# Kernel optimization log

Hardware: AMD Instinct MI355X
Metric: run time of the kernel (lower is better)

The kernel has to match this reference:

```python
import jax, jax.numpy as jnp
import numpy as np

N_EMBD, N_HEAD, N_KV_HEAD = 1024, 16, 4
HEAD_DIM = N_EMBD // N_HEAD  # 64
VE_GATE_CH = 12
RMS_EPS = 1.1920929e-07  # torch fp32 finfo.eps (F.rms_norm default)


def setup_inputs() -> dict:
    key = jax.random.key(0)
    ks = jax.random.split(key, 8)
    B, S = 2, 2048
    x = jax.random.normal(ks[0], (B, S, N_EMBD), dtype=jnp.float32)
    ve = jax.random.normal(ks[1], (B, S, N_KV_HEAD * HEAD_DIM), dtype=jnp.float32)
    # RoPE cache
    half = HEAD_DIM // 2
    inv_freq = 1.0 / (10000.0 ** (np.arange(half, dtype=np.float32) / half))
    ang = np.arange(S, dtype=np.float32)[:, None] * inv_freq[None, :]  # [S, 32]
    cos = jnp.asarray(np.cos(ang))[:, None, :]  # [S,1,32]
    sin = jnp.asarray(np.sin(ang))[:, None, :]
    attention_mask = jnp.ones((B, S), dtype=jnp.int32)
    sc = 0.02
    Wq = sc * jax.random.normal(ks[2], (N_EMBD, N_EMBD), dtype=jnp.float32)
    Wk = sc * jax.random.normal(ks[3], (N_KV_HEAD * HEAD_DIM, N_EMBD), dtype=jnp.float32)
    Wv = sc * jax.random.normal(ks[4], (N_KV_HEAD * HEAD_DIM, N_EMBD), dtype=jnp.float32)
    Wproj = sc * jax.random.normal(ks[5], (N_EMBD, N_EMBD), dtype=jnp.float32)
    Wgate = sc * jax.random.normal(ks[6], (N_KV_HEAD, VE_GATE_CH), dtype=jnp.float32)
    return {"x": x, "ve": ve, "cos": cos, "sin": sin,
            "Wq": Wq, "Wk": Wk, "Wv": Wv, "Wproj": Wproj, "Wgate": Wgate,
            "attention_mask": attention_mask, "left_window": 1024}


def _rope(t, cos, sin):
    half = t.shape[-1] // 2
    t1, t2 = t[..., :half], t[..., half:]
    return jnp.concatenate([t1 * cos + t2 * sin, -t1 * sin + t2 * cos], axis=-1)


def _rms_norm(t):
    return t * jax.lax.rsqrt(jnp.mean(t * t, axis=-1, keepdims=True) + RMS_EPS)


def reference(x, ve, cos, sin, Wq, Wk, Wv, Wproj, Wgate, attention_mask, left_window):
    B, S, _ = x.shape
    q = (x @ Wq.T).reshape(B, S, N_HEAD, HEAD_DIM)
    k = (x @ Wk.T).reshape(B, S, N_KV_HEAD, HEAD_DIM)
    v = (x @ Wv.T).reshape(B, S, N_KV_HEAD, HEAD_DIM)
    # value-embedding gating: 3*sigmoid(linear(x[..., :12])) per kv head
    gate = 3.0 * jax.nn.sigmoid(x[..., :VE_GATE_CH] @ Wgate.T)  # [B,S,Hkv]
    v = v + gate[..., None] * ve.reshape(B, S, N_KV_HEAD, HEAD_DIM)
    q = _rms_norm(_rope(q, cos, sin)) * 1.2
    k = _rms_norm(_rope(k, cos, sin)) * 1.2
    q = q.transpose(0, 2, 1, 3)  # [B,H,S,hd]
    k = k.transpose(0, 2, 1, 3)  # [B,Hkv,S,hd]
    v = v.transpose(0, 2, 1, 3)
    rep = N_HEAD // N_KV_HEAD
    k = jnp.repeat(k, rep, axis=1)  # repeat_interleave over head dim
    v = jnp.repeat(v, rep, axis=1)
    # causal + sliding-window bias, materialized as in the original
    pos = jnp.arange(S)
    allowed = (pos[:, None] >= pos[None, :]) & ((pos[:, None] - pos[None, :]) < left_window)
    allowed = allowed[None, None] & attention_mask.astype(bool)[:, None, None, :]  # [B,1,S,S]
    neg = jnp.finfo(x.dtype).min
    bias = jnp.where(allowed, jnp.float32(0.0), neg).astype(x.dtype)
    scale = 1.0 / np.sqrt(HEAD_DIM)
    scores = jnp.einsum('bhqd,bhkd->bhqk', q, k) * scale + bias
    w = jax.nn.softmax(scores, axis=-1)
    y = jnp.einsum('bhqk,bhkd->bhqd', w, v)
    y = y.transpose(0, 2, 1, 3).reshape(B, S, N_EMBD)
    return y @ Wproj.T
```

## Files before the change

kernel.cpp:

```cpp
#include <hip/hip_runtime.h>
#include <hip/hip_bf16.h>

#define SS 2048
#define EE 1024
#define RMS_EPS 1.1920929e-07f

typedef short v8s __attribute__((ext_vector_type(8)));
typedef float v4f __attribute__((ext_vector_type(4)));

#define MFMA16 __builtin_amdgcn_mfma_f32_16x16x32_bf16

__device__ __forceinline__ ushort f2bf(float f){
    union { __hip_bfloat16 b; ushort u; } c; c.b = __float2bfloat16(f); return c.u;
}
__device__ __forceinline__ float bf2f(ushort u){
    union { uint u; float f; } c; c.u = ((uint)u) << 16; return c.f;
}
__device__ __forceinline__ void split8(const float* p, uint4& H, uint4& L){
    float4 a = *(const float4*)p, b = *(const float4*)(p+4);
    float v[8] = {a.x,a.y,a.z,a.w,b.x,b.y,b.z,b.w};
    ushort hs[8], ls[8];
#pragma unroll
    for (int e=0;e<8;e++){
        ushort h = f2bf(v[e]);
        hs[e] = h;
        ls[e] = f2bf(v[e] - bf2f(h));
    }
    H = *(uint4*)hs; L = *(uint4*)ls;
}

__global__ __launch_bounds__(256)
void split_pre(const float* __restrict__ s, ushort* __restrict__ dh,
               ushort* __restrict__ dl, int n8)
{
    int i = blockIdx.x*256 + threadIdx.x;
    if (i < n8){
        uint4 H, L;
        split8(s + (size_t)i*8, H, L);
        *(uint4*)(dh + (size_t)i*8) = H;
        *(uint4*)(dl + (size_t)i*8) = L;
    }
}

template<bool PRE>
__global__ __launch_bounds__(256)
void qkv_kernel(const float* __restrict__ x, const float* __restrict__ ve,
                const float* __restrict__ Wq, const float* __restrict__ Wk,
                const float* __restrict__ Wv, const float* __restrict__ Wg,
                const ushort* __restrict__ xh, const ushort* __restrict__ xl,
                const ushort* __restrict__ Wch, const ushort* __restrict__ Wcl,
                const float* __restrict__ cosb, const float* __restrict__ sinb,
                ushort* __restrict__ qhb, ushort* __restrict__ qlb,
                ushort* __restrict__ khb, ushort* __restrict__ klb,
                ushort* __restrict__ vhT, ushort* __restrict__ vlT)
{
    __shared__ ushort Axh[128*64];
    __shared__ ushort Axl[128*64];
    __shared__ ushort Bwh[64*64];
    __shared__ ushort Bwl[64*64];
    const int t = threadIdx.x;
    const int lane = t & 63, w = t >> 6;
    const int g = lane >> 4, ln = lane & 15;
    const int nt = blockIdx.x, mt = blockIdx.y;
    const float* W;
    if (nt < 16)      W = Wq + (size_t)nt*64*EE;
    else if (nt < 20) W = Wk + (size_t)(nt-16)*64*EE;
    else              W = Wv + (size_t)(nt-20)*64*EE;
    const v4f vzero = {0.f,0.f,0.f,0.f};
    v4f acc[2][4];
#pragma unroll
    for (int m=0;m<2;m++)
#pragma unroll
        for (int j=0;j<4;j++) acc[m][j] = vzero;

    const int sr = t>>3, sc = t&7;
    for (int kt = 0; kt < EE; kt += 64){
#pragma unroll
        for (int p2=0;p2<4;p2++){
            int rr = sr + 32*p2;
            int off = rr*64 + ((sc ^ (rr&7))<<3);
            if (PRE){
                *(uint4*)&Axh[off] = *(const uint4*)(xh + (size_t)(mt*128+rr)*EE + kt + sc*8);
                *(uint4*)&Axl[off] = *(const uint4*)(xl + (size_t)(mt*128+rr)*EE + kt + sc*8);
            } else {
                uint4 H,L; split8(x + (size_t)(mt*128+rr)*EE + kt + sc*8, H, L);
                *(uint4*)&Axh[off] = H; *(uint4*)&Axl[off] = L;
            }
        }
#pragma unroll
        for (int p2=0;p2<2;p2++){
            int rr = sr + 32*p2;
            int off = rr*64 + ((sc ^ (rr&7))<<3);
            if (PRE){
                *(uint4*)&Bwh[off] = *(const uint4*)(Wch + (size_t)(nt*64+rr)*EE + kt + sc*8);
                *(uint4*)&Bwl[off] = *(const uint4*)(Wcl + (size_t)(nt*64+rr)*EE + kt + sc*8);
            } else {
                uint4 H,L; split8(W + (size_t)rr*EE + kt + sc*8, H, L);
                *(uint4*)&Bwh[off] = H; *(uint4*)&Bwl[off] = L;
            }
        }
        __syncthreads();
        v8s ah[2][2], al[2][2], bh[4][2], bl[4][2];
#pragma unroll
        for (int m=0;m<2;m++){
            int row = 32*w + 16*m + ln;
#pragma unroll
            for (int s=0;s<2;s++){
                int off = row*64 + (((4*s+g) ^ (row&7))<<3);
                ah[m][s] = *(v8s*)&Axh[off];
                al[m][s] = *(v8s*)&Axl[off];
            }
        }
#pragma unroll
        for (int j=0;j<4;j++){
            int row = 16*j + ln;
#pragma unroll
            for (int s=0;s<2;s++){
                int off = row*64 + (((4*s+g) ^ (row&7))<<3);
                bh[j][s] = *(v8s*)&Bwh[off];
                bl[j][s] = *(v8s*)&Bwl[off];
            }
        }
#pragma unroll
        for (int m=0;m<2;m++)
#pragma unroll
            for (int j=0;j<4;j++)
#pragma unroll
                for (int s=0;s<2;s++){
                    acc[m][j] = MFMA16(ah[m][s], bh[j][s], acc[m][j], 0,0,0);
                    acc[m][j] = MFMA16(ah[m][s], bl[j][s], acc[m][j], 0,0,0);
                    acc[m][j] = MFMA16(al[m][s], bh[j][s], acc[m][j], 0,0,0);
                }
        __syncthreads();
    }

#pragma unroll
    for (int m=0;m<2;m++){
#pragma unroll
        for (int r=0;r<4;r++){
            int srow = mt*128 + 32*w + 16*m + 4*g + r;
            int bb  = srow >> 11;
            int ss_ = srow & 2047;
            float v0 = acc[m][0][r], v1 = acc[m][1][r];
            float v2 = acc[m][2][r], v3 = acc[m][3][r];
            if (nt < 20){
                float c0 = cosb[ss_*32 + ln],      s0 = sinb[ss_*32 + ln];
                float c1 = cosb[ss_*32 + 16 + ln], s1 = sinb[ss_*32 + 16 + ln];
                float lo0 =  v0*c0 + v2*s0, hi0 = -v0*s0 + v2*c0;
                float lo1 =  v1*c1 + v3*s1, hi1 = -v1*s1 + v3*c1;
                float ssq = lo0*lo0 + hi0*hi0 + lo1*lo1 + hi1*hi1;
                ssq += __shfl_xor(ssq, 1); ssq += __shfl_xor(ssq, 2);
                ssq += __shfl_xor(ssq, 4); ssq += __shfl_xor(ssq, 8);
                float rs = rsqrtf(ssq*(1.f/64.f) + RMS_EPS) * 1.2f;
                size_t base = (nt < 16) ? ((size_t)(bb*16 + nt)*SS + ss_)*64
                                        : ((size_t)(bb*4 + (nt-16))*SS + ss_)*64;
                ushort* dh = (nt < 16) ? (qhb + base) : (khb + base);
                ushort* dl = (nt < 16) ? (qlb + base) : (klb + base);
                float o0 = lo0*rs, o1 = lo1*rs, o2 = hi0*rs, o3 = hi1*rs;
                ushort h0 = f2bf(o0), h1 = f2bf(o1), h2 = f2bf(o2), h3 = f2bf(o3);
                dh[ln]    = h0; dl[ln]    = f2bf(o0 - bf2f(h0));
                dh[16+ln] = h1; dl[16+ln] = f2bf(o1 - bf2f(h1));
                dh[32+ln] = h2; dl[32+ln] = f2bf(o2 - bf2f(h2));
                dh[48+ln] = h3; dl[48+ln] = f2bf(o3 - bf2f(h3));
            } else {
                int head = nt - 20;
                float gsum = 0.f;
                const float* xr = x + (size_t)srow * EE;
#pragma unroll
                for (int c = 0; c < 12; c++) gsum += xr[c] * Wg[head*12 + c];
                float gate = 3.f / (1.f + __expf(-gsum));
                const float* ver = ve + (size_t)srow*256 + head*64;
                size_t vbase = ((size_t)(bb*4 + head)*64)*SS + ss_;
                float dv[4] = {v0, v1, v2, v3};
#pragma unroll
                for (int j=0;j<4;j++){
                    int d = 16*j + ln;
                    float ov = dv[j] + gate*ver[d];
                    ushort hh = f2bf(ov);
                    vhT[vbase + (size_t)d*SS] = hh;
                    vlT[vbase + (size_t)d*SS] = f2bf(ov - bf2f(hh));
                }
            }
        }
    }
}

__global__ __launch_bounds__(256)
void attn_kernel(const ushort* __restrict__ qhb, const ushort* __restrict__ qlb,
                 const ushort* __restrict__ khb, const ushort* __restrict__ klb,
                 const ushort* __restrict__ vhT, const ushort* __restrict__ vlT,
                 const int* __restrict__ amask, const int* __restrict__ lwp,
                 ushort* __restrict__ yhb, ushort* __restrict__ ylb)
{
    __shared__ ushort SMEM[16384];
    __shared__ float mbias[64];
    ushort* Kh = SMEM;
    ushort* Kl = SMEM + 4096;
    ushort* Vh = SMEM + 8192;
    ushort* Vl = SMEM + 12288;
    const int t = threadIdx.x, lane = t & 63, w = t >> 6;
    const int g = lane >> 4, ln = lane & 15;
    const int qt = blockIdx.x, bh = blockIdx.y;
    const int b = bh >> 4, h = bh & 15, kvh = h >> 2;
    const int LW = lwp[0];
    const int q0 = qt*64;
    const ushort* Qhp = qhb + ((size_t)(b*16+h)*SS + q0)*64;
    const ushort* Qlp = qlb + ((size_t)(b*16+h)*SS + q0)*64;
    const ushort* Khp = khb + ((size_t)(b*4+kvh)*SS)*64;
    const ushort* Klp = klb + ((size_t)(b*4+kvh)*SS)*64;
    const ushort* Vhp = vhT + (size_t)(b*4+kvh)*64*SS;
    const ushort* Vlp = vlT + (size_t)(b*4+kvh)*64*SS;

    v8s qfh[2], qfl[2];
    {
        int row = 16*w + ln;
#pragma unroll
        for (int s=0;s<2;s++){
            qfh[s] = *(const v8s*)(Qhp + (size_t)row*64 + (4*s+g)*8);
            qfl[s] = *(const v8s*)(Qlp + (size_t)row*64 + (4*s+g)*8);
        }
    }
    const int qg = q0 + 16*w + ln;
    const int keyk = (ln&3) ^ ((ln>>2)<<1);
    float m_r = -1e30f, l_r = 0.f;
    const v4f vzero = {0.f,0.f,0.f,0.f};
    v4f o[4];
#pragma unroll
    for (int dt=0;dt<4;dt++) o[dt] = vzero;

    const int sr = t>>3, sc = t&7;
    int lo = q0 - LW + 1; if (lo < 0) lo = 0;
    for (int kt = lo>>6; kt <= qt; kt++){
        int k0 = kt*64;
        __syncthreads();
#pragma unroll
        for (int p2=0;p2<2;p2++){
            int rr = sr + 32*p2;
            int kkey = (rr&3) ^ (((rr>>3)&3)<<1);
            int koff = rr*64 + ((sc ^ kkey)<<3);
            *(uint4*)&Kh[koff] = *(const uint4*)(Khp + (size_t)(k0+rr)*64 + sc*8);
            *(uint4*)&Kl[koff] = *(const uint4*)(Klp + (size_t)(k0+rr)*64 + sc*8);
            int voff = rr*64 + ((sc ^ (rr&7))<<3);
            *(uint4*)&Vh[voff] = *(const uint4*)(Vhp + (size_t)rr*SS + k0 + sc*8);
            *(uint4*)&Vl[voff] = *(const uint4*)(Vlp + (size_t)rr*SS + k0 + sc*8);
        }
        if (t < 64) mbias[t] = amask[(b<<11) + k0 + t] ? 0.f : -3.0e38f;
        __syncthreads();

        float p[4][4];
#pragma unroll
        for (int tau=0;tau<4;tau++){
            v4f sa = vzero;
            int krow = 32*(tau&1) + 8*(ln>>2) + 4*(tau>>1) + (ln&3);
#pragma unroll
            for (int s=0;s<2;s++){
                int off = krow*64 + (((4*s+g) ^ keyk)<<3);
                v8s afh = *(v8s*)&Kh[off];
                v8s afl = *(v8s*)&Kl[off];
                sa = MFMA16(afh, qfh[s], sa, 0,0,0);
                sa = MFMA16(afh, qfl[s], sa, 0,0,0);
                sa = MFMA16(afl, qfh[s], sa, 0,0,0);
            }
#pragma unroll
            for (int r=0;r<4;r++) p[tau][r] = sa[r];
        }

        float pmax = -3.0e38f;
#pragma unroll
        for (int tau=0;tau<4;tau++)
#pragma unroll
            for (int r=0;r<4;r++){
                int kk  = 32*(tau&1) + 8*g + 4*(tau>>1) + r;
                int kgl = k0 + kk;
                float scv = p[tau][r]*0.125f + mbias[kk];
                bool ok = (kgl <= qg) && (qg - kgl < LW);
                scv = ok ? scv : -3.0e38f;
                p[tau][r] = scv;
                pmax = fmaxf(pmax, scv);
            }
        pmax = fmaxf(pmax, __shfl_xor(pmax,16));
        pmax = fmaxf(pmax, __shfl_xor(pmax,32));
        float mnew = fmaxf(m_r, pmax);
        float al = __expf(m_r - mnew);
        float ls = 0.f;
#pragma unroll
        for (int tau=0;tau<4;tau++)
#pragma unroll
            for (int r=0;r<4;r++){
                float e = __expf(p[tau][r] - mnew);
                p[tau][r] = e; ls += e;
            }
        ls += __shfl_xor(ls,16); ls += __shfl_xor(ls,32);
        m_r = mnew; l_r = l_r*al + ls;

        v8s pbh[2], pbl[2];
#pragma unroll
        for (int s=0;s<2;s++){
            v8s ph, pl;
#pragma unroll
            for (int e=0;e<8;e++){
                float val = p[2*(e>>2)+s][e&3];
                ushort hh = f2bf(val);
                ph[e] = (short)hh;
                pl[e] = (short)f2bf(val - bf2f(hh));
            }
            pbh[s]=ph; pbl[s]=pl;
        }
#pragma unroll
        for (int dt=0;dt<4;dt++){
            o[dt] = o[dt]*al;
            int drow = 16*dt + ln;
#pragma unroll
            for (int s=0;s<2;s++){
                int off = drow*64 + (((4*s+g) ^ (ln&7))<<3);
                v8s vfh = *(v8s*)&Vh[off];
                v8s vfl = *(v8s*)&Vl[off];
                o[dt] = MFMA16(vfh, pbh[s], o[dt], 0,0,0);
                o[dt] = MFMA16(vfh, pbl[s], o[dt], 0,0,0);
                o[dt] = MFMA16(vfl, pbh[s], o[dt], 0,0,0);
            }
        }
    }

    __syncthreads();
    float inv = (l_r > 0.f) ? (1.0f / l_r) : 0.f;
    float* Ot = (float*)SMEM;
#pragma unroll
    for (int dt=0;dt<4;dt++)
#pragma unroll
        for (int r=0;r<4;r++){
            int d = 16*dt + 4*g + r;
            Ot[d*68 + 16*w + ln] = o[dt][r]*inv;
        }
    __syncthreads();
    {
        int q = t>>2, dp = t&3;
        ushort th[16], tl[16];
#pragma unroll
        for (int i=0;i<16;i++){
            float val = Ot[(dp*16+i)*68 + q];
            ushort hh = f2bf(val);
            th[i] = hh;
            tl[i] = f2bf(val - bf2f(hh));
        }
        size_t doff = (size_t)(b*SS + q0 + q)*EE + h*64 + dp*16;
        *(uint4*)(yhb + doff)     = *(uint4*)&th[0];
        *(uint4*)(yhb + doff + 8) = *(uint4*)&th[8];
        *(uint4*)(ylb + doff)     = *(uint4*)&tl[0];
        *(uint4*)(ylb + doff + 8) = *(uint4*)&tl[8];
    }
}

template<bool PRE>
__global__ __launch_bounds__(256)
void proj_kernel(const ushort* __restrict__ yhb, const ushort* __restrict__ ylb,
                 const float* __restrict__ Wp, const ushort* __restrict__ Wph,
                 const ushort* __restrict__ Wpl, float* __restrict__ out)
{
    __shared__ ushort Ayh[128*64];
    __shared__ ushort Ayl[128*64];
    __shared__ ushort Bh[64*64];
    __shared__ ushort Bl[64*64];
    const int t = threadIdx.x;
    const int lane = t & 63, w = t >> 6;
    const int g = lane >> 4, ln = lane & 15;
    const int nt = blockIdx.x, mt = blockIdx.y;
    const v4f vzero = {0.f,0.f,0.f,0.f};
    v4f acc[2][4];
#pragma unroll
    for (int m=0;m<2;m++)
#pragma unroll
        for (int j=0;j<4;j++) acc[m][j] = vzero;

    const int sr = t>>3, sc = t&7;
    for (int kt = 0; kt < EE; kt += 64){
#pragma unroll
        for (int p2=0;p2<4;p2++){
            int rr = sr + 32*p2;
            int off = rr*64 + ((sc ^ (rr&7))<<3);
            *(uint4*)&Ayh[off] = *(const uint4*)(yhb + (size_t)(mt*128+rr)*EE + kt + sc*8);
            *(uint4*)&Ayl[off] = *(const uint4*)(ylb + (size_t)(mt*128+rr)*EE + kt + sc*8);
        }
#pragma unroll
        for (int p2=0;p2<2;p2++){
            int rr = sr + 32*p2;
            int off = rr*64 + ((sc ^ (rr&7))<<3);
            if (PRE){
                *(uint4*)&Bh[off] = *(const uint4*)(Wph + (size_t)(nt*64+rr)*EE + kt + sc*8);
                *(uint4*)&Bl[off] = *(const uint4*)(Wpl + (size_t)(nt*64+rr)*EE + kt + sc*8);
            } else {
                uint4 H,L; split8(Wp + (size_t)(nt*64+rr)*EE + kt + sc*8, H, L);
                *(uint4*)&Bh[off] = H; *(uint4*)&Bl[off] = L;
            }
        }
        __syncthreads();
        v8s ah[2][2], al[2][2], bh[4][2], bl[4][2];
#pragma unroll
        for (int m=0;m<2;m++){
            int row = 32*w + 16*m + ln;
#pragma unroll
            for (int s=0;s<2;s++){
                int off = row*64 + (((4*s+g) ^ (row&7))<<3);
                ah[m][s] = *(v8s*)&Ayh[off];
                al[m][s] = *(v8s*)&Ayl[off];
            }
        }
#pragma unroll
        for (int j=0;j<4;j++){
            int row = 16*j + ln;
#pragma unroll
            for (int s=0;s<2;s++){
                int off = row*64 + (((4*s+g) ^ (row&7))<<3);
                bh[j][s] = *(v8s*)&Bh[off];
                bl[j][s] = *(v8s*)&Bl[off];
            }
        }
#pragma unroll
        for (int m=0;m<2;m++)
#pragma unroll
            for (int j=0;j<4;j++)
#pragma unroll
                for (int s=0;s<2;s++){
                    acc[m][j] = MFMA16(ah[m][s], bh[j][s], acc[m][j], 0,0,0);
                    acc[m][j] = MFMA16(ah[m][s], bl[j][s], acc[m][j], 0,0,0);
                    acc[m][j] = MFMA16(al[m][s], bh[j][s], acc[m][j], 0,0,0);
                }
        __syncthreads();
    }

#pragma unroll
    for (int m=0;m<2;m++)
#pragma unroll
        for (int r=0;r<4;r++){
            size_t grow = (size_t)mt*128 + 32*w + 16*m + 4*g + r;
#pragma unroll
            for (int j=0;j<4;j++)
                out[grow*EE + nt*64 + 16*j + ln] = acc[m][j][r];
        }
}

extern "C" void kernel_launch(void* const* d_in, const int* in_sizes, int n_in,
                              void* d_out, int out_size, void* d_ws, size_t ws_size,
                              hipStream_t stream)
{
    (void)in_sizes; (void)n_in; (void)out_size;
    const float* x     = (const float*)d_in[0];
    const float* ve    = (const float*)d_in[1];
    const float* cosb  = (const float*)d_in[2];
    const float* sinb  = (const float*)d_in[3];
    const float* Wq    = (const float*)d_in[4];
    const float* Wk    = (const float*)d_in[5];
    const float* Wv    = (const float*)d_in[6];
    const float* Wp    = (const float*)d_in[7];
    const float* Wg    = (const float*)d_in[8];
    const int*   amask = (const int*)d_in[9];
    const int*   lw    = (const int*)d_in[10];
    float* out = (float*)d_out;
    char* ws = (char*)d_ws;

    if (ws_size >= (size_t)(50u<<20)){
        ushort* xh  = (ushort*)(ws);
        ushort* xl  = (ushort*)(ws + ( 8u<<20));
        ushort* Wch = (ushort*)(ws + (16u<<20));
        ushort* Wcl = (ushort*)(ws + (19u<<20));
        ushort* Wph = (ushort*)(ws + (22u<<20));
        ushort* Wpl = (ushort*)(ws + (24u<<20));
        ushort* qhb = (ushort*)(ws + (26u<<20));
        ushort* qlb = (ushort*)(ws + (34u<<20));
        ushort* khb = (ushort*)(ws + (42u<<20));
        ushort* klb = (ushort*)(ws + (44u<<20));
        ushort* vhT = (ushort*)(ws + (46u<<20));
        ushort* vlT = (ushort*)(ws + (48u<<20));
        ushort* yhb = xh;
        ushort* ylb = xl;

        split_pre<<<2048, 256, 0, stream>>>(x,  xh,  xl,  524288);
        split_pre<<< 512, 256, 0, stream>>>(Wq, Wch, Wcl, 131072);
        split_pre<<< 128, 256, 0, stream>>>(Wk, Wch + (size_t)1024*EE, Wcl + (size_t)1024*EE, 32768);
        split_pre<<< 128, 256, 0, stream>>>(Wv, Wch + (size_t)1280*EE, Wcl + (size_t)1280*EE, 32768);
        split_pre<<< 512, 256, 0, stream>>>(Wp, Wph, Wpl, 131072);

        qkv_kernel<true><<<dim3(24,32), 256, 0, stream>>>(x, ve, Wq, Wk, Wv, Wg,
                xh, xl, Wch, Wcl, cosb, sinb, qhb, qlb, khb, klb, vhT, vlT);
        attn_kernel<<<dim3(32,32), 256, 0, stream>>>(qhb, qlb, khb, klb, vhT, vlT,
                amask, lw, yhb, ylb);
        proj_kernel<true><<<dim3(16,32), 256, 0, stream>>>(yhb, ylb, Wp, Wph, Wpl, out);
    } else {
        ushort* qhb = (ushort*)(ws);
        ushort* qlb = (ushort*)(ws + ( 8u<<20));
        ushort* khb = (ushort*)(ws + (16u<<20));
        ushort* klb = (ushort*)(ws + (18u<<20));
        ushort* vhT = (ushort*)(ws + (20u<<20));
        ushort* vlT = (ushort*)(ws + (22u<<20));
        ushort* yhb = (ushort*)(ws + (24u<<20));
        ushort* ylb = (ushort*)(ws + (32u<<20));

        qkv_kernel<false><<<dim3(24,32), 256, 0, stream>>>(x, ve, Wq, Wk, Wv, Wg,
                nullptr, nullptr, nullptr, nullptr, cosb, sinb,
                qhb, qlb, khb, klb, vhT, vlT);
        attn_kernel<<<dim3(32,32), 256, 0, stream>>>(qhb, qlb, khb, klb, vhT, vlT,
                amask, lw, yhb, ylb);
        proj_kernel<false><<<dim3(16,32), 256, 0, stream>>>(yhb, ylb, Wp, nullptr, nullptr, out);
    }
}
```

Before: 265.2 us.

## Fuse split launches, prefetch K/V tiles, lazy softmax rescale in attention

Merges the five fp32-to-bf16 hi/lo split launches into one kernel, cutting launch overhead. In the attention kernel, the next K/V tile and mask are loaded into registers while the current tile is processed, hiding global load latency. Causal/window masking is now applied only on edge tiles. The softmax uses exp2 with a pre-scaled log2e constant and skips rescaling the accumulator unless the running max grows by more than a threshold. It also adds an occupancy hint through launch bounds, which raises register pressure from the prefetch buffers and risks spills.

```diff
diff --git a/kernel.cpp b/kernel.cpp
--- a/kernel.cpp
+++ b/kernel.cpp
@@ -30,16 +30,30 @@
 }
 
 __global__ __launch_bounds__(256)
-void split_pre(const float* __restrict__ s, ushort* __restrict__ dh,
-               ushort* __restrict__ dl, int n8)
+void split_all(const float* __restrict__ x,  const float* __restrict__ Wq,
+               const float* __restrict__ Wk, const float* __restrict__ Wv,
+               const float* __restrict__ Wp,
+               ushort* __restrict__ xh,  ushort* __restrict__ xl,
+               ushort* __restrict__ Wch, ushort* __restrict__ Wcl,
+               ushort* __restrict__ Wph, ushort* __restrict__ Wpl)
 {
     int i = blockIdx.x*256 + threadIdx.x;
-    if (i < n8){
-        uint4 H, L;
-        split8(s + (size_t)i*8, H, L);
-        *(uint4*)(dh + (size_t)i*8) = H;
-        *(uint4*)(dl + (size_t)i*8) = L;
-    }
+    const float* s; ushort *dh, *dl; size_t off;
+    if (i < 524288){
+        s = x; dh = xh; dl = xl; off = (size_t)i*8;
+    } else if (i < 655360){
+        size_t j = i - 524288; s = Wq; dh = Wch; dl = Wcl; off = j*8;
+    } else if (i < 688128){
+        size_t j = i - 655360; s = Wk; dh = Wch + (size_t)1024*EE; dl = Wcl + (size_t)1024*EE; off = j*8;
+    } else if (i < 720896){
+        size_t j = i - 688128; s = Wv; dh = Wch + (size_t)1280*EE; dl = Wcl + (size_t)1280*EE; off = j*8;
+    } else {
+        size_t j = i - 720896; s = Wp; dh = Wph; dl = Wpl; off = j*8;
+    }
+    uint4 H, L;
+    split8(s + off, H, L);
+    *(uint4*)(dh + off) = H;
+    *(uint4*)(dl + off) = L;
 }
 
 template<bool PRE>
@@ -185,7 +199,7 @@
     }
 }
 
-__global__ __launch_bounds__(256)
+__global__ __launch_bounds__(256, 4)
 void attn_kernel(const ushort* __restrict__ qhb, const ushort* __restrict__ qlb,
                  const ushort* __restrict__ khb, const ushort* __restrict__ klb,
                  const ushort* __restrict__ vhT, const ushort* __restrict__ vlT,
@@ -230,21 +244,45 @@
 
     const int sr = t>>3, sc = t&7;
     int lo = q0 - LW + 1; if (lo < 0) lo = 0;
-    for (int kt = lo>>6; kt <= qt; kt++){
+    const int kt0 = lo>>6;
+    const float SC2 = 0.125f * 1.44269504088896f;
+
+    uint4 rkh[2], rkl[2], rvh[2], rvl[2];
+    int mb = 0;
+#pragma unroll
+    for (int p2=0;p2<2;p2++){
+        int rr = sr + 32*p2;
+        rkh[p2] = *(const uint4*)(Khp + (size_t)(kt0*64+rr)*64 + sc*8);
+        rkl[p2] = *(const uint4*)(Klp + (size_t)(kt0*64+rr)*64 + sc*8);
+        rvh[p2] = *(const uint4*)(Vhp + (size_t)rr*SS + kt0*64 + sc*8);
+        rvl[p2] = *(const uint4*)(Vlp + (size_t)rr*SS + kt0*64 + sc*8);
+    }
+    if (t < 64) mb = amask[(b<<11) + kt0*64 + t];
+
+    for (int kt = kt0; kt <= qt; kt++){
         int k0 = kt*64;
         __syncthreads();
 #pragma unroll
         for (int p2=0;p2<2;p2++){
             int rr = sr + 32*p2;
             int kkey = (rr&3) ^ (((rr>>3)&3)<<1);
-            int koff = rr*64 + ((sc ^ kkey)<<3);
-            *(uint4*)&Kh[koff] = *(const uint4*)(Khp + (size_t)(k0+rr)*64 + sc*8);
-            *(uint4*)&Kl[koff] = *(const uint4*)(Klp + (size_t)(k0+rr)*64 + sc*8);
-            int voff = rr*64 + ((sc ^ (rr&7))<<3);
-            *(uint4*)&Vh[voff] = *(const uint4*)(Vhp + (size_t)rr*SS + k0 + sc*8);
-            *(uint4*)&Vl[voff] = *(const uint4*)(Vlp + (size_t)rr*SS + k0 + sc*8);
-        }
-        if (t < 64) mbias[t] = amask[(b<<11) + k0 + t] ? 0.f : -3.0e38f;
+            *(uint4*)&Kh[rr*64 + ((sc ^ kkey)<<3)] = rkh[p2];
+            *(uint4*)&Kl[rr*64 + ((sc ^ kkey)<<3)] = rkl[p2];
+            *(uint4*)&Vh[rr*64 + ((sc ^ (rr&7))<<3)] = rvh[p2];
+            *(uint4*)&Vl[rr*64 + ((sc ^ (rr&7))<<3)] = rvl[p2];
+        }
+        if (t < 64) mbias[t] = mb ? 0.f : -3.0e38f;
+        if (kt < qt){
+#pragma unroll
+            for (int p2=0;p2<2;p2++){
+                int rr = sr + 32*p2;
+                rkh[p2] = *(const uint4*)(Khp + (size_t)(k0+64+rr)*64 + sc*8);
+                rkl[p2] = *(const uint4*)(Klp + (size_t)(k0+64+rr)*64 + sc*8);
+                rvh[p2] = *(const uint4*)(Vhp + (size_t)rr*SS + k0+64 + sc*8);
+                rvl[p2] = *(const uint4*)(Vlp + (size_t)rr*SS + k0+64 + sc*8);
+            }
+            if (t < 64) mb = amask[(b<<11) + k0+64 + t];
+        }
         __syncthreads();
 
         float p[4][4];
@@ -265,33 +303,43 @@
             for (int r=0;r<4;r++) p[tau][r] = sa[r];
         }
 
+        const bool edge = (kt == qt) || (k0 < q0 + 64 - LW);
         float pmax = -3.0e38f;
 #pragma unroll
         for (int tau=0;tau<4;tau++)
 #pragma unroll
             for (int r=0;r<4;r++){
                 int kk  = 32*(tau&1) + 8*g + 4*(tau>>1) + r;
-                int kgl = k0 + kk;
-                float scv = p[tau][r]*0.125f + mbias[kk];
-                bool ok = (kgl <= qg) && (qg - kgl < LW);
-                scv = ok ? scv : -3.0e38f;
+                float scv = p[tau][r]*SC2 + mbias[kk];
+                if (edge){
+                    int kgl = k0 + kk;
+                    bool ok = (kgl <= qg) && (qg - kgl < LW);
+                    scv = ok ? scv : -3.0e38f;
+                }
                 p[tau][r] = scv;
                 pmax = fmaxf(pmax, scv);
             }
         pmax = fmaxf(pmax, __shfl_xor(pmax,16));
         pmax = fmaxf(pmax, __shfl_xor(pmax,32));
-        float mnew = fmaxf(m_r, pmax);
-        float al = __expf(m_r - mnew);
+        bool defer = __all(pmax <= m_r + 8.0f);
+        float mnew = defer ? m_r : fmaxf(m_r, pmax);
         float ls = 0.f;
 #pragma unroll
         for (int tau=0;tau<4;tau++)
 #pragma unroll
             for (int r=0;r<4;r++){
-                float e = __expf(p[tau][r] - mnew);
+                float e = exp2f(p[tau][r] - mnew);
                 p[tau][r] = e; ls += e;
             }
         ls += __shfl_xor(ls,16); ls += __shfl_xor(ls,32);
-        m_r = mnew; l_r = l_r*al + ls;
+        if (!defer){
+            float al = exp2f(m_r - mnew);
+            l_r = l_r*al;
+#pragma unroll
+            for (int dt=0;dt<4;dt++) o[dt] = o[dt]*al;
+            m_r = mnew;
+        }
+        l_r += ls;
 
         v8s pbh[2], pbl[2];
 #pragma unroll
@@ -308,7 +356,6 @@
         }
 #pragma unroll
         for (int dt=0;dt<4;dt++){
-            o[dt] = o[dt]*al;
             int drow = 16*dt + ln;
 #pragma unroll
             for (int s=0;s<2;s++){
@@ -474,12 +521,8 @@
         ushort* yhb = xh;
         ushort* ylb = xl;
 
-        split_pre<<<2048, 256, 0, stream>>>(x,  xh,  xl,  524288);
-        split_pre<<< 512, 256, 0, stream>>>(Wq, Wch, Wcl, 131072);
-        split_pre<<< 128, 256, 0, stream>>>(Wk, Wch + (size_t)1024*EE, Wcl + (size_t)1024*EE, 32768);
-        split_pre<<< 128, 256, 0, stream>>>(Wv, Wch + (size_t)1280*EE, Wcl + (size_t)1280*EE, 32768);
-        split_pre<<< 512, 256, 0, stream>>>(Wp, Wph, Wpl, 131072);
-
+        split_all<<<3328, 256, 0, stream>>>(x, Wq, Wk, Wv, Wp,
+                                            xh, xl, Wch, Wcl, Wph, Wpl);
         qkv_kernel<true><<<dim3(24,32), 256, 0, stream>>>(x, ve, Wq, Wk, Wv, Wg,
                 xh, xl, Wch, Wcl, cosb, sinb, qhb, qlb, khb, klb, vhT, vlT);
         attn_kernel<<<dim3(32,32), 256, 0, stream>>>(qhb, qlb, khb, klb, vhT, vlT,
```

Result: slower. 354.3 us (+33.6%).
